# Kernel optimization log

Measured on AMD Instinct MI355X. Metric: run time of the kernel, lower is better.

Reference implementation:

```python
import jax, jax.numpy as jnp
import numpy as np

B, T, D, H, DFF = 2, 2048, 1024, 16, 4096
K = D // H  # head size = 64
EPS = 1e-5


def _layernorm(x, g, b):
    mu = jnp.mean(x, axis=-1, keepdims=True)
    var = jnp.mean(jnp.square(x - mu), axis=-1, keepdims=True)
    return (x - mu) * jax.lax.rsqrt(var + EPS) * g + b


def setup_inputs() -> dict:
    key = jax.random.key(0)
    ks = jax.random.split(key, 12)
    s_attn = 1.0 / np.sqrt(D)
    s_ff1 = 1.0 / np.sqrt(D)
    s_ff2 = 1.0 / np.sqrt(DFF)
    return {
        "x": jax.random.normal(ks[0], (B, T, D), jnp.float32),
        # per-head q/k/v projections, stacked: [H, D, K] (each head's Linear has no bias)
        "Wq": jax.random.normal(ks[1], (H, D, K), jnp.float32) * s_attn,
        "Wk": jax.random.normal(ks[2], (H, D, K), jnp.float32) * s_attn,
        "Wv": jax.random.normal(ks[3], (H, D, K), jnp.float32) * s_attn,
        "Wo": jax.random.normal(ks[4], (D, D), jnp.float32) * s_attn,
        "bo": jax.random.normal(ks[5], (D,), jnp.float32) * 0.01,
        "W1": jax.random.normal(ks[6], (D, DFF), jnp.float32) * s_ff1,
        "b1": jax.random.normal(ks[7], (DFF,), jnp.float32) * 0.01,
        "W2": jax.random.normal(ks[8], (DFF, D), jnp.float32) * s_ff2,
        "b2": jax.random.normal(ks[9], (D,), jnp.float32) * 0.01,
        "g1": jnp.ones((D,), jnp.float32),
        "be1": jnp.zeros((D,), jnp.float32),
        "g2": jnp.ones((D,), jnp.float32),
        "be2": jnp.zeros((D,), jnp.float32),
    }


def reference(x, Wq, Wk, Wv, Wo, bo, W1, b1, W2, b2, g1, be1, g2, be2):
    b, t, d = x.shape
    h = _layernorm(x, g1, be1)
    # multi-head attention (per-head linear projections, fused via einsum)
    q = jnp.einsum('btd,hdk->bhtk', h, Wq)
    k = jnp.einsum('btd,hdk->bhtk', h, Wk)
    v = jnp.einsum('btd,hdk->bhtk', h, Wv)
    scores = jnp.einsum('bhtk,bhsk->bhts', q, k) * (K ** -0.5)
    causal = jnp.tril(jnp.ones((t, t), bool))
    scores = jnp.where(causal, scores, -jnp.inf)
    attn = jax.nn.softmax(scores, axis=-1)
    o = jnp.einsum('bhts,bhsk->bhtk', attn, v)
    o = o.transpose(0, 2, 1, 3).reshape(b, t, d)  # concat heads
    x = x + o @ Wo + bo
    # feed-forward (exact GELU, as torch default)
    h2 = _layernorm(x, g2, be2)
    ff = jax.nn.gelu(h2 @ W1 + b1, approximate=False) @ W2 + b2
    return x + ff
```

## Files before the change

kernel.cpp:

```cpp
#include <hip/hip_runtime.h>
#include <hip/hip_bf16.h>


#define BT   4096
#define DIM  1024
#define DFF  4096
#define TSEQ 2048
#define NHEAD 16
#define HDIM 64
#define QKV_LD 3072

typedef __attribute__((ext_vector_type(8))) short  bf16x8;
typedef __attribute__((ext_vector_type(4))) float  floatx4;

__device__ __forceinline__ void async_copy16(const __hip_bfloat16* g, __hip_bfloat16* l) {
    __builtin_amdgcn_global_load_lds(
        (const __attribute__((address_space(1))) void*)g,
        (__attribute__((address_space(3))) void*)l, 16, 0, 0);
}

__device__ __forceinline__ floatx4 mfma_bf16(bf16x8 a, bf16x8 b, floatx4 c) {
    return __builtin_amdgcn_mfma_f32_16x16x32_bf16(a, b, c, 0, 0, 0);
}

__global__ __launch_bounds__(256) void ln_kernel(const float* __restrict__ x,
                                                 const float* __restrict__ g,
                                                 const float* __restrict__ be,
                                                 __hip_bfloat16* __restrict__ out) {
    const int row = blockIdx.x;
    const int t = threadIdx.x;
    const float4 v = ((const float4*)(x + (size_t)row * DIM))[t];
    float s  = v.x + v.y + v.z + v.w;
    float ss = v.x * v.x + v.y * v.y + v.z * v.z + v.w * v.w;
    for (int d = 1; d < 64; d <<= 1) { s += __shfl_xor(s, d); ss += __shfl_xor(ss, d); }
    __shared__ float red[8];
    const int w = t >> 6;
    if ((t & 63) == 0) { red[w] = s; red[w + 4] = ss; }
    __syncthreads();
    s  = red[0] + red[1] + red[2] + red[3];
    ss = red[4] + red[5] + red[6] + red[7];
    const float mu = s * (1.0f / DIM);
    const float rstd = rsqrtf(ss * (1.0f / DIM) - mu * mu + 1e-5f);
    const float4 gv = ((const float4*)g)[t];
    const float4 bv = ((const float4*)be)[t];
    __hip_bfloat16* o = out + (size_t)row * DIM + t * 4;
    o[0] = __float2bfloat16((v.x - mu) * rstd * gv.x + bv.x);
    o[1] = __float2bfloat16((v.y - mu) * rstd * gv.y + bv.y);
    o[2] = __float2bfloat16((v.z - mu) * rstd * gv.z + bv.z);
    o[3] = __float2bfloat16((v.w - mu) * rstd * gv.w + bv.w);
}

__global__ __launch_bounds__(256) void transpose_cast(const float* __restrict__ src, int src_ld,
                                                      __hip_bfloat16* __restrict__ dst, int dst_ld) {
    __shared__ float tile[64][65];
    const int r0 = blockIdx.x * 64, c0 = blockIdx.y * 64;
    const int tr = threadIdx.x >> 6;
    const int tc = threadIdx.x & 63;
    for (int i = 0; i < 16; ++i) {
        const int r = i * 4 + tr;
        tile[r][tc] = src[(size_t)(r0 + r) * src_ld + c0 + tc];
    }
    __syncthreads();
    for (int i = 0; i < 16; ++i) {
        const int c = i * 4 + tr;
        dst[(size_t)(c0 + c) * dst_ld + r0 + tc] = __float2bfloat16(tile[tc][c]);
    }
}

__global__ __launch_bounds__(256) void transpose_qkv(const float* __restrict__ Wq,
                                                     const float* __restrict__ Wk,
                                                     const float* __restrict__ Wv,
                                                     __hip_bfloat16* __restrict__ dst) {
    __shared__ float tile[64][65];
    const int hz = blockIdx.y;
    const int proj = hz >> 4, h = hz & 15;
    const float* W = (proj == 0 ? Wq : (proj == 1 ? Wk : Wv)) + (size_t)h * DIM * HDIM;
    const int r0 = blockIdx.x * 64;
    const int tr = threadIdx.x >> 6;
    const int tc = threadIdx.x & 63;
    for (int i = 0; i < 16; ++i) {
        const int r = i * 4 + tr;
        tile[r][tc] = W[(size_t)(r0 + r) * HDIM + tc];
    }
    __syncthreads();
    for (int i = 0; i < 16; ++i) {
        const int k = i * 4 + tr;
        dst[(size_t)(proj * 1024 + h * 64 + k) * DIM + r0 + tc] = __float2bfloat16(tile[tc][k]);
    }
}

__global__ __launch_bounds__(256) void transpose_v(const __hip_bfloat16* __restrict__ qkv,
                                                   __hip_bfloat16* __restrict__ vt) {
    __shared__ __align__(16) __hip_bfloat16 tile[64 * 72];
    const int t = threadIdx.x;
    const int bh = blockIdx.y;
    const int b = bh >> 4, h = bh & 15;
    const int t0 = blockIdx.x * 64;
    const __hip_bfloat16* src = qkv + (size_t)b * TSEQ * QKV_LD + 2048 + h * HDIM;
    const int lo = t >> 3, k8 = t & 7;
    for (int i = 0; i < 2; ++i) {
        const int rr = i * 32 + lo;
        const bf16x8 v = *(const bf16x8*)(src + (size_t)(t0 + rr) * QKV_LD + k8 * 8);
        const int cb = k8 ^ ((rr >> 3) & 7);
        *(bf16x8*)(tile + rr * 72 + cb * 8) = v;
    }
    __syncthreads();
    for (int i = 0; i < 2; ++i) {
        const int dd = i * 32 + lo;
        const int c0 = dd >> 3, cl = dd & 7;
        bf16x8 o;
        for (int jj = 0; jj < 8; ++jj) {
            const int key = k8 * 8 + jj;
            o[jj] = *(const short*)(tile + key * 72 + (c0 ^ ((key >> 3) & 7)) * 8 + cl);
        }
        *(bf16x8*)(vt + ((size_t)bh * HDIM + dd) * TSEQ + t0 + k8 * 8) = o;
    }
}

template <int EPI>
__global__ __launch_bounds__(256) void gemm_bt(const __hip_bfloat16* __restrict__ A,
                                               const __hip_bfloat16* __restrict__ Bt,
                                               __hip_bfloat16* __restrict__ outb,
                                               const float* __restrict__ bias,
                                               int M, int N, int K) {
    __shared__ __align__(16) __hip_bfloat16 As[128 * 32];
    __shared__ __align__(16) __hip_bfloat16 Bs[128 * 32];
    const int t = threadIdx.x;
    const int w = t >> 6, l = t & 63;
    const int quad = l >> 4, tl = l & 15;
    const int wr = w >> 1, wc = w & 1;
    const int m0 = blockIdx.y * 128, n0 = blockIdx.x * 128;

    floatx4 acc[4][4] = {};
    const int rowA = t >> 2;
    const int c8 = (t & 3) << 3;

    for (int k0 = 0; k0 < K; k0 += 32) {
        __syncthreads();
        {
            const __hip_bfloat16* gA = A + (size_t)(m0 + rowA) * K + k0 + c8;
            const __hip_bfloat16* gB = Bt + (size_t)(n0 + rowA) * K + k0 + c8;
            async_copy16(gA,                  As + w * 512);
            async_copy16(gA + (size_t)64 * K, As + 2048 + w * 512);
            async_copy16(gB,                  Bs + w * 512);
            async_copy16(gB + (size_t)64 * K, Bs + 2048 + w * 512);
        }
        __syncthreads();

        bf16x8 af[4], bfr[4];
        const int aRow = wr * 64 + tl;
        const int bRow = wc * 64 + tl;
        for (int mi = 0; mi < 4; ++mi)
            af[mi] = *(const bf16x8*)(As + (aRow + mi * 16) * 32 + quad * 8);
        for (int ni = 0; ni < 4; ++ni)
            bfr[ni] = *(const bf16x8*)(Bs + (bRow + ni * 16) * 32 + quad * 8);
        for (int mi = 0; mi < 4; ++mi)
            for (int ni = 0; ni < 4; ++ni)
                acc[mi][ni] = mfma_bf16(af[mi], bfr[ni], acc[mi][ni]);
    }

    const int rowBase = m0 + wr * 64 + quad * 4;
    const int colBase = n0 + wc * 64 + tl;
    for (int mi = 0; mi < 4; ++mi) {
        for (int ni = 0; ni < 4; ++ni) {
            const int c = colBase + ni * 16;
            for (int j = 0; j < 4; ++j) {
                const int r = rowBase + mi * 16 + j;
                const size_t idx = (size_t)r * N + c;
                float v = acc[mi][ni][j];
                if (EPI == 1) {
                    v += bias[c];
                    v = 0.5f * v * (1.0f + erff(v * 0.70710678118654752f));
                }
                outb[idx] = __float2bfloat16(v);
            }
        }
    }
}

__global__ __launch_bounds__(256) void gemm_bt_n64(const __hip_bfloat16* __restrict__ A,
                                                   const __hip_bfloat16* __restrict__ Bt,
                                                   float* __restrict__ outf,
                                                   const float* __restrict__ bias,
                                                   const float* __restrict__ resid,
                                                   int M, int N, int K) {
    __shared__ __align__(16) __hip_bfloat16 As[128 * 32];
    __shared__ __align__(16) __hip_bfloat16 Bs[64 * 32];
    const int t = threadIdx.x;
    const int w = t >> 6, l = t & 63;
    const int quad = l >> 4, tl = l & 15;
    const int m0 = blockIdx.y * 128, n0 = blockIdx.x * 64;

    floatx4 acc[2][4] = {};
    const int rowA = t >> 2;
    const int c8 = (t & 3) << 3;

    for (int k0 = 0; k0 < K; k0 += 32) {
        __syncthreads();
        {
            const __hip_bfloat16* gA = A + (size_t)(m0 + rowA) * K + k0 + c8;
            const __hip_bfloat16* gB = Bt + (size_t)(n0 + rowA) * K + k0 + c8;
            async_copy16(gA,                  As + w * 512);
            async_copy16(gA + (size_t)64 * K, As + 2048 + w * 512);
            async_copy16(gB,                  Bs + w * 512);
        }
        __syncthreads();

        bf16x8 af[2], bfr[4];
        for (int mi = 0; mi < 2; ++mi)
            af[mi] = *(const bf16x8*)(As + (w * 32 + mi * 16 + tl) * 32 + quad * 8);
        for (int ni = 0; ni < 4; ++ni)
            bfr[ni] = *(const bf16x8*)(Bs + (ni * 16 + tl) * 32 + quad * 8);
        for (int mi = 0; mi < 2; ++mi)
            for (int ni = 0; ni < 4; ++ni)
                acc[mi][ni] = mfma_bf16(af[mi], bfr[ni], acc[mi][ni]);
    }

    const int rowBase = m0 + w * 32 + quad * 4;
    const int colBase = n0 + tl;
    for (int mi = 0; mi < 2; ++mi) {
        for (int ni = 0; ni < 4; ++ni) {
            const int c = colBase + ni * 16;
            for (int j = 0; j < 4; ++j) {
                const int r = rowBase + mi * 16 + j;
                const size_t idx = (size_t)r * N + c;
                outf[idx] = resid[idx] + acc[mi][ni][j] + bias[c];
            }
        }
    }
}

#define KS_LD 72
#define VT_LD 72
#define PL_LD 72
__global__ __launch_bounds__(256) void attn_kernel(const __hip_bfloat16* __restrict__ qkv,
                                                   const __hip_bfloat16* __restrict__ vt,
                                                   __hip_bfloat16* __restrict__ out) {
    __shared__ __align__(16) __hip_bfloat16 Ks[64 * KS_LD];
    __shared__ __align__(16) __hip_bfloat16 Vts[64 * VT_LD];
    __shared__ __align__(16) __hip_bfloat16 Pl[4][16 * PL_LD];
    const int t = threadIdx.x;
    const int w = t >> 6, l = t & 63;
    const int quad = l >> 4, tl = l & 15;
    const int id = blockIdx.x;
    const int bh = ((id & 7) << 2) | ((id >> 3) & 3);
    const int pq = id >> 5;
    const int b = bh >> 4, h = bh & 15;
    const __hip_bfloat16* Qp  = qkv + (size_t)b * TSEQ * QKV_LD + h * HDIM;
    const __hip_bfloat16* Kp  = Qp + 1024;
    const __hip_bfloat16* Vtp = vt + (size_t)bh * HDIM * TSEQ;
    __hip_bfloat16* P = Pl[w];
    const float cscale = 0.125f * 1.4426950408889634f;
    const int srow = t >> 3, sk8 = t & 7;

    for (int half = 0; half < 2; ++half) {
        const int qb = half ? (31 - pq) : pq;
        const int qw = qb * 64 + w * 16;
        const int nb = qb + 1;

        const __hip_bfloat16* qrow = Qp + (size_t)(qw + tl) * QKV_LD + quad * 8;
        const bf16x8 qf0 = *(const bf16x8*)qrow;
        const bf16x8 qf1 = *(const bf16x8*)(qrow + 32);
        floatx4 oacc[4] = {};
        float l_i[4] = {0.0f, 0.0f, 0.0f, 0.0f};
        const int myrow = quad * 4;

        for (int it = 0; it < nb; ++it) {
            const int s0 = it * 64;
            __syncthreads();
            for (int i = 0; i < 2; ++i) {
                const int rr = i * 32 + srow;
                const bf16x8 kv = *(const bf16x8*)(Kp  + (size_t)(s0 + rr) * QKV_LD + sk8 * 8);
                const bf16x8 vv = *(const bf16x8*)(Vtp + (size_t)rr * TSEQ + s0 + sk8 * 8);
                *(bf16x8*)(Ks  + rr * KS_LD + sk8 * 8) = kv;
                *(bf16x8*)(Vts + rr * VT_LD + sk8 * 8) = vv;
            }
            __syncthreads();

            floatx4 sc[4];
            for (int ni = 0; ni < 4; ++ni) {
                const __hip_bfloat16* kr = Ks + (ni * 16 + tl) * KS_LD + quad * 8;
                floatx4 z = {0.0f, 0.0f, 0.0f, 0.0f};
                z = mfma_bf16(qf0, *(const bf16x8*)kr, z);
                sc[ni] = mfma_bf16(qf1, *(const bf16x8*)(kr + 32), z);
            }

            const bool lastB = (it == nb - 1);
            for (int ni = 0; ni < 4; ++ni) {
                const int keyrel = ni * 16 + tl - w * 16;
                for (int j = 0; j < 4; ++j) {
                    float pv = exp2f(sc[ni][j] * cscale);
                    if (lastB && keyrel > myrow + j) pv = 0.0f;
                    l_i[j] += pv;
                    P[(myrow + j) * PL_LD + ni * 16 + tl] = __float2bfloat16(pv);
                }
            }
            __builtin_amdgcn_wave_barrier();

            for (int kc = 0; kc < 2; ++kc) {
                const bf16x8 pf = *(const bf16x8*)(P + tl * PL_LD + kc * 32 + quad * 8);
                for (int ni = 0; ni < 4; ++ni) {
                    const bf16x8 vf = *(const bf16x8*)(Vts + (ni * 16 + tl) * VT_LD
                                                       + kc * 32 + quad * 8);
                    oacc[ni] = mfma_bf16(pf, vf, oacc[ni]);
                }
            }
        }

        for (int d = 1; d < 16; d <<= 1) {
            float r0 = __shfl_xor(l_i[0], d), r1 = __shfl_xor(l_i[1], d);
            float r2 = __shfl_xor(l_i[2], d), r3 = __shfl_xor(l_i[3], d);
            l_i[0] += r0; l_i[1] += r1; l_i[2] += r2; l_i[3] += r3;
        }
        for (int j = 0; j < 4; ++j) {
            const float inv = 1.0f / l_i[j];
            const int rg = qw + quad * 4 + j;
            __hip_bfloat16* orow = out + ((size_t)b * TSEQ + rg) * DIM + h * HDIM;
            for (int ni = 0; ni < 4; ++ni)
                orow[ni * 16 + tl] = __float2bfloat16(oacc[ni][j] * inv);
        }
    }
}

extern "C" void kernel_launch(void* const* d_in, const int* in_sizes, int n_in,
                              void* d_out, int out_size, void* d_ws, size_t ws_size,
                              hipStream_t stream) {
    const float* x   = (const float*)d_in[0];
    const float* Wq  = (const float*)d_in[1];
    const float* Wk  = (const float*)d_in[2];
    const float* Wv  = (const float*)d_in[3];
    const float* Wo  = (const float*)d_in[4];
    const float* bo  = (const float*)d_in[5];
    const float* W1  = (const float*)d_in[6];
    const float* b1  = (const float*)d_in[7];
    const float* W2  = (const float*)d_in[8];
    const float* b2  = (const float*)d_in[9];
    const float* g1  = (const float*)d_in[10];
    const float* be1 = (const float*)d_in[11];
    const float* g2  = (const float*)d_in[12];
    const float* be2 = (const float*)d_in[13];
    float* out = (float*)d_out;

    size_t off = 0;
    char* wsb = (char*)d_ws;
    auto carve = [&](size_t bytes) {
        void* p = wsb + off;
        off += (bytes + 255) & ~(size_t)255;
        return p;
    };
    __hip_bfloat16* WqkvT = (__hip_bfloat16*)carve((size_t)3072 * 1024 * 2);
    __hip_bfloat16* WoT   = (__hip_bfloat16*)carve((size_t)1024 * 1024 * 2);
    __hip_bfloat16* W1T   = (__hip_bfloat16*)carve((size_t)4096 * 1024 * 2);
    __hip_bfloat16* W2T   = (__hip_bfloat16*)carve((size_t)1024 * 4096 * 2);
    __hip_bfloat16* h1    = (__hip_bfloat16*)carve((size_t)BT * DIM * 2);
    __hip_bfloat16* qkv   = (__hip_bfloat16*)carve((size_t)BT * QKV_LD * 2);
    __hip_bfloat16* vtb   = (__hip_bfloat16*)carve((size_t)BT * DIM * 2);
    __hip_bfloat16* att   = (__hip_bfloat16*)carve((size_t)BT * DIM * 2);
    float*          x2    = (float*)carve((size_t)BT * DIM * 4);
    __hip_bfloat16* h2    = (__hip_bfloat16*)carve((size_t)BT * DIM * 2);
    __hip_bfloat16* ff1   = (__hip_bfloat16*)carve((size_t)BT * DFF * 2);

    transpose_qkv<<<dim3(16, 48), 256, 0, stream>>>(Wq, Wk, Wv, WqkvT);
    transpose_cast<<<dim3(16, 16), 256, 0, stream>>>(Wo, 1024, WoT, 1024);
    transpose_cast<<<dim3(16, 64), 256, 0, stream>>>(W1, 4096, W1T, 1024);
    transpose_cast<<<dim3(64, 16), 256, 0, stream>>>(W2, 1024, W2T, 4096);

    ln_kernel<<<BT, 256, 0, stream>>>(x, g1, be1, h1);
    gemm_bt<0><<<dim3(24, 32), 256, 0, stream>>>(h1, WqkvT, qkv, nullptr, BT, QKV_LD, DIM);
    transpose_v<<<dim3(32, 32), 256, 0, stream>>>(qkv, vtb);
    attn_kernel<<<512, 256, 0, stream>>>(qkv, vtb, att);
    gemm_bt_n64<<<dim3(16, 32), 256, 0, stream>>>(att, WoT, x2, bo, x, BT, DIM, DIM);
    ln_kernel<<<BT, 256, 0, stream>>>(x2, g2, be2, h2);
    gemm_bt<1><<<dim3(32, 32), 256, 0, stream>>>(h2, W1T, ff1, b1, BT, DFF, DIM);
    gemm_bt_n64<<<dim3(16, 32), 256, 0, stream>>>(ff1, W2T, out, b2, x2, BT, DIM, DFF);
}
```

Measured before the change: 404.9 us.

## Deepen K tile to 64 with XOR-swizzled LDS and XCD-aware block mapping

The N=64 output GEMMs (Wo projection and W2 down-projection) now stage 64-wide K slices instead of 32, which halves the number of barrier pairs per K sweep. The LDS layout uses an XOR swizzle on 16-byte chunks to avoid bank conflicts on the wider rows. A 1D grid remaps blocks so that each XCD gets a contiguous band of M rows, meant to improve L2 reuse of the A tiles. LDS per block doubles, which may lower occupancy, and loads are still not double-buffered.

```diff
diff --git a/kernel.cpp b/kernel.cpp
--- a/kernel.cpp
+++ b/kernel.cpp
@@ -178,42 +178,54 @@
     }
 }
 
-__global__ __launch_bounds__(256) void gemm_bt_n64(const __hip_bfloat16* __restrict__ A,
+__global__ __launch_bounds__(256) void gemm_bt_k64(const __hip_bfloat16* __restrict__ A,
                                                    const __hip_bfloat16* __restrict__ Bt,
                                                    float* __restrict__ outf,
                                                    const float* __restrict__ bias,
                                                    const float* __restrict__ resid,
                                                    int M, int N, int K) {
-    __shared__ __align__(16) __hip_bfloat16 As[128 * 32];
-    __shared__ __align__(16) __hip_bfloat16 Bs[64 * 32];
+    __shared__ __align__(16) __hip_bfloat16 As[128 * 64];
+    __shared__ __align__(16) __hip_bfloat16 Bs[64 * 64];
     const int t = threadIdx.x;
     const int w = t >> 6, l = t & 63;
     const int quad = l >> 4, tl = l & 15;
-    const int m0 = blockIdx.y * 128, n0 = blockIdx.x * 64;
+    const int id = blockIdx.x;
+    const int xcd = id & 7, jb = id >> 3;
+    const int n0 = (jb & 15) * 64;
+    const int m0 = ((jb >> 4) * 8 + xcd) * 128;
 
     floatx4 acc[2][4] = {};
-    const int rowA = t >> 2;
-    const int c8 = (t & 3) << 3;
-
-    for (int k0 = 0; k0 < K; k0 += 32) {
+    const int srow = t >> 3;
+    const int scg  = t & 7;
+
+    for (int k0 = 0; k0 < K; k0 += 64) {
         __syncthreads();
-        {
-            const __hip_bfloat16* gA = A + (size_t)(m0 + rowA) * K + k0 + c8;
-            const __hip_bfloat16* gB = Bt + (size_t)(n0 + rowA) * K + k0 + c8;
-            async_copy16(gA,                  As + w * 512);
-            async_copy16(gA + (size_t)64 * K, As + 2048 + w * 512);
-            async_copy16(gB,                  Bs + w * 512);
+        for (int i = 0; i < 4; ++i) {
+            const int row = i * 32 + srow;
+            async_copy16(A + (size_t)(m0 + row) * K + k0 + ((scg ^ (row & 7)) << 3),
+                         As + i * 2048 + w * 512);
+        }
+        for (int i = 0; i < 2; ++i) {
+            const int row = i * 32 + srow;
+            async_copy16(Bt + (size_t)(n0 + row) * K + k0 + ((scg ^ (row & 7)) << 3),
+                         Bs + i * 2048 + w * 512);
         }
         __syncthreads();
 
-        bf16x8 af[2], bfr[4];
-        for (int mi = 0; mi < 2; ++mi)
-            af[mi] = *(const bf16x8*)(As + (w * 32 + mi * 16 + tl) * 32 + quad * 8);
-        for (int ni = 0; ni < 4; ++ni)
-            bfr[ni] = *(const bf16x8*)(Bs + (ni * 16 + tl) * 32 + quad * 8);
-        for (int mi = 0; mi < 2; ++mi)
-            for (int ni = 0; ni < 4; ++ni)
-                acc[mi][ni] = mfma_bf16(af[mi], bfr[ni], acc[mi][ni]);
+        for (int ks = 0; ks < 2; ++ks) {
+            bf16x8 af[2], bfr[4];
+            for (int mi = 0; mi < 2; ++mi) {
+                const int r = w * 32 + mi * 16 + tl;
+                af[mi] = *(const bf16x8*)(As + r * 64 + (((ks * 4 + quad) ^ (r & 7)) << 3));
+            }
+            for (int ni = 0; ni < 4; ++ni) {
+                const int r = ni * 16 + tl;
+                bfr[ni] = *(const bf16x8*)(Bs + r * 64 + (((ks * 4 + quad) ^ (r & 7)) << 3));
+            }
+            for (int mi = 0; mi < 2; ++mi)
+                for (int ni = 0; ni < 4; ++ni)
+                    acc[mi][ni] = mfma_bf16(af[mi], bfr[ni], acc[mi][ni]);
+        }
     }
 
     const int rowBase = m0 + w * 32 + quad * 4;
@@ -369,8 +381,8 @@
     gemm_bt<0><<<dim3(24, 32), 256, 0, stream>>>(h1, WqkvT, qkv, nullptr, BT, QKV_LD, DIM);
     transpose_v<<<dim3(32, 32), 256, 0, stream>>>(qkv, vtb);
     attn_kernel<<<512, 256, 0, stream>>>(qkv, vtb, att);
-    gemm_bt_n64<<<dim3(16, 32), 256, 0, stream>>>(att, WoT, x2, bo, x, BT, DIM, DIM);
+    gemm_bt_k64<<<512, 256, 0, stream>>>(att, WoT, x2, bo, x, BT, DIM, DIM);
     ln_kernel<<<BT, 256, 0, stream>>>(x2, g2, be2, h2);
     gemm_bt<1><<<dim3(32, 32), 256, 0, stream>>>(h2, W1T, ff1, b1, BT, DFF, DIM);
-    gemm_bt_n64<<<dim3(16, 32), 256, 0, stream>>>(ff1, W2T, out, b2, x2, BT, DIM, DFF);
-}
+    gemm_bt_k64<<<512, 256, 0, stream>>>(ff1, W2T, out, b2, x2, BT, DIM, DFF);
+}
```

Result: faster. 385.4 us (-4.8%).
